# Kernel optimization log

Measured on AMD Instinct MI355X. Metric: run time of the kernel, lower is better.

## Reference

```python
import jax, jax.numpy as jnp
import numpy as np

H = 768
NH = 12
HD = 64
R = 4
SCALING = 8.0 / 4.0  # lora_alpha / r


def setup_inputs() -> dict:
    key = jax.random.key(0)
    ks = jax.random.split(key, 16)
    B, T = 16, 512
    s = 0.02
    x = jax.random.normal(ks[0], (B, T, H), dtype=jnp.float32)
    mask = jax.random.randint(ks[1], (B, T), 0, 2, dtype=jnp.int32)
    return {
        "x": x,
        "mask": mask,
        "Wq": jax.random.normal(ks[2], (H, H), jnp.float32) * s,
        "bq": jnp.zeros((H,), jnp.float32),
        "Aq": jax.random.normal(ks[3], (R, H), jnp.float32) * s,
        "Bq": jax.random.normal(ks[4], (H, R), jnp.float32) * s,
        "Wk": jax.random.normal(ks[5], (H, H), jnp.float32) * s,
        "bk": jnp.zeros((H,), jnp.float32),
        "Wv": jax.random.normal(ks[6], (H, H), jnp.float32) * s,
        "bv": jnp.zeros((H,), jnp.float32),
        "Av": jax.random.normal(ks[7], (R, H), jnp.float32) * s,
        "Bv": jax.random.normal(ks[8], (H, R), jnp.float32) * s,
        "Wo": jax.random.normal(ks[9], (H, H), jnp.float32) * s,
        "bo": jnp.zeros((H,), jnp.float32),
    }


def _lora_linear(x, W, b, A, Bm):
    # base: x @ W^T + b ; lora: (x @ A^T) @ B^T * scaling (dropout inactive at eval)
    return x @ W.T + b + (x @ A.T) @ Bm.T * SCALING


def reference(x, mask, Wq, bq, Aq, Bq, Wk, bk, Wv, bv, Av, Bv, Wo, bo):
    B, T, _ = x.shape
    q = _lora_linear(x, Wq, bq, Aq, Bq).reshape(B, T, NH, HD).transpose(0, 2, 1, 3)
    k = (x @ Wk.T + bk).reshape(B, T, NH, HD).transpose(0, 2, 1, 3)
    v = _lora_linear(x, Wv, bv, Av, Bv).reshape(B, T, NH, HD).transpose(0, 2, 1, 3)
    # [B, NH, T, T]
    scores = jnp.einsum("bhqd,bhkd->bhqk", q, k) / jnp.sqrt(jnp.float32(HD))
    m = (mask == 0)[:, None, None, :]  # mask key positions where mask==0
    scores = jnp.where(m, jnp.float32(-1e9), scores)
    attn = jax.nn.softmax(scores, axis=-1)  # dropout inactive at eval
    out = jnp.einsum("bhqk,bhkd->bhqd", attn, v)
    out = out.transpose(0, 2, 1, 3).reshape(B, T, H)
    return out @ Wo.T + bo
```

## Files before the change

### kernel.cpp

```cpp
#include <hip/hip_runtime.h>
#include <stdint.h>

#define H 768
#define NHEAD 12
#define HDIM 64
#define BATCH 16
#define TSEQ 512
#define BT (BATCH*TSEQ)
#define C3 (3*H)
#define LDQK 1536

typedef __attribute__((ext_vector_type(8))) short short8;
typedef __attribute__((ext_vector_type(4))) float floatx4;
typedef unsigned short u16;

__device__ __forceinline__ u16 f2bf(float f) {
    union { float f; unsigned int u; } v; v.f = f;
    unsigned int u = v.u;
    return (u16)((u + 0x7FFFu + ((u >> 16) & 1u)) >> 16);
}

__device__ __forceinline__ void async_ld16(const void* g, void* l) {
    __builtin_amdgcn_global_load_lds((__attribute__((address_space(1))) void*)g,
                                     (__attribute__((address_space(3))) void*)l,
                                     16, 0, 0);
}

#define PREP_BLOCKS 9216
#define CVT_BLOCKS  6144
#define CMP_BLOCKS  16
__global__ void prep_kernel(const float* __restrict__ Wq, const float* __restrict__ bq,
                            const float* __restrict__ Aq, const float* __restrict__ Bq,
                            const float* __restrict__ Wk, const float* __restrict__ bk,
                            const float* __restrict__ Wv, const float* __restrict__ bv,
                            const float* __restrict__ Av, const float* __restrict__ Bv,
                            const float* __restrict__ Wo, const float* __restrict__ x,
                            const int* __restrict__ mask,
                            u16* __restrict__ Wall, u16* __restrict__ Wobf,
                            float* __restrict__ bias_all, u16* __restrict__ xb,
                            u16* __restrict__ tokl, int* __restrict__ nvalid)
{
    const int bid = blockIdx.x;
    if (bid >= PREP_BLOCKS + CVT_BLOCKS) {
        const int b = bid - (PREP_BLOCKS + CVT_BLOCKS);
        if (threadIdx.x >= 64) return;
        const int lane = threadIdx.x;
        int base = 0;
        for (int t0 = 0; t0 < TSEQ; t0 += 64) {
            const int mv = mask[b*TSEQ + t0 + lane];
            const unsigned long long bal = __ballot(mv != 0);
            if (mv != 0) {
                const int pre = __popcll(bal & ((1ull << lane) - 1ull));
                tokl[b*TSEQ + base + pre] = (u16)(t0 + lane);
            }
            base += __popcll(bal);
        }
        if (lane == 0) nvalid[b] = base;
        for (int i = base + lane; i < TSEQ; i += 64) tokl[b*TSEQ + i] = 0;
        return;
    }
    if (bid >= PREP_BLOCKS) {
        const int i = ((bid - PREP_BLOCKS) * 256 + threadIdx.x) * 4;
        const float4 v = *(const float4*)(x + i);
        u16 o[4] = { f2bf(v.x), f2bf(v.y), f2bf(v.z), f2bf(v.w) };
        *(uint2*)(xb + i) = *(const uint2*)o;
        return;
    }
    const int idx = bid * 256 + threadIdx.x;
    const int r = idx / H;
    const int c = idx - r * H;
    if (r < H) {
        float v = Wq[idx] + 2.0f * (Bq[r*4+0]*Aq[c] + Bq[r*4+1]*Aq[H+c] +
                                    Bq[r*4+2]*Aq[2*H+c] + Bq[r*4+3]*Aq[3*H+c]);
        Wall[idx] = f2bf(v);
    } else if (r < 2*H) {
        Wall[idx] = f2bf(Wk[idx - H*H]);
    } else if (r < 3*H) {
        const int rr = r - 2*H;
        float v = Wv[rr*H + c] + 2.0f * (Bv[rr*4+0]*Av[c] + Bv[rr*4+1]*Av[H+c] +
                                         Bv[rr*4+2]*Av[2*H+c] + Bv[rr*4+3]*Av[3*H+c]);
        Wall[idx] = f2bf(v);
    } else {
        Wobf[idx - 3*H*H] = f2bf(Wo[idx - 3*H*H]);
    }
    if (idx < C3) {
        bias_all[idx] = (idx < H) ? bq[idx] : (idx < 2*H ? bk[idx - H] : bv[idx - 2*H]);
    }
}

template<int MODE, int TM, int NB, int MB, int MAP, int GB>
__global__ __launch_bounds__(256)
void gemm_bt(const u16* __restrict__ A, const u16* __restrict__ Bw,
             const float* __restrict__ bias, void* __restrict__ Cout,
             const u16* __restrict__ tokl, const int* __restrict__ nvalid,
             int K, int ldc)
{
    constexpr int MT = TM / 32;
    __shared__ u16 Ablk[TM * 64];
    __shared__ u16 Bblk[128 * 64];
    const int tid  = threadIdx.x;
    const int wave = tid >> 6;
    const int lane = tid & 63;
    const int quad = lane >> 4;
    const int l16  = lane & 15;

    int m0, n0;
    {
        const int j   = blockIdx.x;
        const int xcd = j & 7;
        const int loc = j >> 3;
        if (MAP == 0) {
            constexpr int Mx = MB / 8;
            const int dm = loc % Mx;
            const int nb = loc / Mx;
            m0 = (xcd + 8*dm) * TM;
            n0 = nb * 128;
        } else {
            const int dm = loc % MB;
            const int nl = loc / MB;
            m0 = dm * TM;
            n0 = (xcd + 8*nl) * 128;
        }
    }

    if (GB) {
        const int b = n0 >> 9;
        if ((n0 & 511) >= ((nvalid[b] + 31) & ~31)) return;
    }

    const int mw = (wave & 1) * (TM / 2);
    const int nw = (wave >> 1) * 64;

    const int r8 = lane >> 3;
    const int kgs = ((lane & 7) ^ r8) * 8;
    const u16* gA = A  + (size_t)(m0 + wave*(TM/4) + r8) * K + kgs;
    const u16* gB = Bw + (size_t)(n0 + wave*32      + r8) * K + kgs;
    const u16* gBp[4];
    if (GB) {
        #pragma unroll
        for (int jj = 0; jj < 4; jj++) {
            const int rb = n0 + wave*32 + jj*8 + r8;
            const int row = (rb & ~511) + (int)tokl[rb];
            gBp[jj] = Bw + (size_t)row * K + kgs;
        }
    }
    u16* lA = Ablk + wave * (TM/4) * 64;
    u16* lB = Bblk + wave * 32 * 64;

    floatx4 acc[MT][4] = {};
    const int sw = l16 & 7;

    for (int k0 = 0; k0 < K; k0 += 64) {
        __syncthreads();
        #pragma unroll
        for (int jj = 0; jj < TM/32; jj++)
            async_ld16(gA + k0 + (size_t)(jj*8) * K, lA + jj*8*64);
        #pragma unroll
        for (int jj = 0; jj < 4; jj++) {
            if (GB) async_ld16(gBp[jj] + k0, lB + jj*8*64);
            else    async_ld16(gB + k0 + (size_t)(jj*8) * K, lB + jj*8*64);
        }
        __syncthreads();
        #pragma unroll
        for (int kk = 0; kk < 2; kk++) {
            short8 af[MT], bfr[4];
            #pragma unroll
            for (int mt = 0; mt < MT; mt++)
                af[mt] = *(const short8*)(Ablk + (mw + mt*16 + l16)*64 + ((quad + 4*kk) ^ sw)*8);
            #pragma unroll
            for (int nt = 0; nt < 4; nt++)
                bfr[nt] = *(const short8*)(Bblk + (nw + nt*16 + l16)*64 + ((quad + 4*kk) ^ sw)*8);
            #pragma unroll
            for (int mt = 0; mt < MT; mt++)
                #pragma unroll
                for (int nt = 0; nt < 4; nt++)
                    acc[mt][nt] = __builtin_amdgcn_mfma_f32_16x16x32_bf16(af[mt], bfr[nt], acc[mt][nt], 0, 0, 0);
        }
    }

    if (MODE == 2) {
        #pragma unroll
        for (int mt = 0; mt < MT; mt++) {
            #pragma unroll
            for (int r = 0; r < 4; r++) {
                const int m  = m0 + mw + mt*16 + quad*4 + r;
                const float bv = bias[m];
                const int hh = m >> 6, d = m & 63;
                #pragma unroll
                for (int nt = 0; nt < 4; nt++) {
                    const int n = n0 + nw + nt*16 + l16;
                    const int b = n >> 9, t = n & 511;
                    ((u16*)Cout)[((size_t)((b*NHEAD + hh)*HDIM + d))*TSEQ + t]
                        = f2bf(acc[mt][nt][r] + bv);
                }
            }
        }
    } else {
        #pragma unroll
        for (int nt = 0; nt < 4; nt++) {
            const int n = n0 + nw + nt*16 + l16;
            const float bv = bias[n];
            #pragma unroll
            for (int mt = 0; mt < MT; mt++) {
                #pragma unroll
                for (int r = 0; r < 4; r++) {
                    const int m = m0 + mw + mt*16 + quad*4 + r;
                    const float v = acc[mt][nt][r] + bv;
                    if (MODE == 1) ((u16*)Cout)[(size_t)m * ldc + n] = f2bf(v);
                    else           ((float*)Cout)[(size_t)m * ldc + n] = v;
                }
            }
        }
    }
}

#define PSTRIDE 40

__global__ __launch_bounds__(256)
void attn_kernel(const u16* __restrict__ qk, const u16* __restrict__ vt,
                 const u16* __restrict__ tokl, const int* __restrict__ nvalid,
                 u16* __restrict__ attn_out)
{
    __shared__ float maskadd[TSEQ];
    __shared__ u16 Kbuf[2][32 * 64];
    __shared__ u16 Vbuf[2][64 * 32];
    __shared__ u16 Pbuf[4][2][16 * PSTRIDE];

    const int qt = blockIdx.x;
    const int bh = blockIdx.y;
    const int b = bh / NHEAD, h = bh - b * NHEAD;
    const int tid  = threadIdx.x;
    const int wave = tid >> 6;
    const int lane = tid & 63;
    const int quad = lane >> 4;
    const int l16  = lane & 15;

    const int nv = nvalid[b];
    const int nt = (nv + 31) >> 5;

    for (int i = tid; i < TSEQ; i += 256)
        maskadd[i] = (i < nv) ? 0.0f : -1e9f;

    const size_t btok = (size_t)b * TSEQ;
    const int q0 = qt * 128 + wave * 32;

    short8 qf[2][2];
    #pragma unroll
    for (int m = 0; m < 2; m++) {
        const u16* qp = qk + (btok + q0 + m*16 + l16) * LDQK + h*HDIM + quad*8;
        qf[m][0] = *(const short8*)qp;
        qf[m][1] = *(const short8*)(qp + 32);
    }

    const u16* vglob = vt + (size_t)bh * HDIM * TSEQ;

    auto stage = [&](int kb, int pp) {
        {
            const int r = lane >> 3;
            const int g = (lane & 7) ^ r;
            const int slot = kb + wave*8 + r;
            const int tk = (int)tokl[btok + slot];
            async_ld16(qk + (btok + tk) * LDQK + H + h*HDIM + g*8,
                       &Kbuf[pp][wave*8*64]);
        }
        {
            const int dr = lane >> 2;
            const int g  = (lane & 3) ^ ((dr >> 1) & 3);
            async_ld16(vglob + (size_t)(wave*16 + dr) * TSEQ + kb + g*8,
                       &Vbuf[pp][wave*16*32]);
        }
    };

    floatx4 o[2][4] = {};
    float lsum[2][4] = {};

    auto compute = [&](int kb, int pp) {
        const u16* Kb_ = Kbuf[pp];
        const u16* Vb_ = Vbuf[pp];
        short8 kf[2][2];
        #pragma unroll
        for (int t = 0; t < 2; t++)
            #pragma unroll
            for (int h2 = 0; h2 < 2; h2++)
                kf[t][h2] = *(const short8*)(Kb_ + (t*16 + l16)*64 + (((h2*4 + quad) ^ (l16 & 7))*8));
        short8 vf[4];
        #pragma unroll
        for (int dt = 0; dt < 4; dt++)
            vf[dt] = *(const short8*)(Vb_ + (dt*16 + l16)*32 + ((quad ^ ((l16 >> 1) & 3))*8));

        floatx4 s[2][2];
        #pragma unroll
        for (int m = 0; m < 2; m++)
            #pragma unroll
            for (int t = 0; t < 2; t++) {
                floatx4 acc = {0.f, 0.f, 0.f, 0.f};
                acc = __builtin_amdgcn_mfma_f32_16x16x32_bf16(qf[m][0], kf[t][0], acc, 0, 0, 0);
                acc = __builtin_amdgcn_mfma_f32_16x16x32_bf16(qf[m][1], kf[t][1], acc, 0, 0, 0);
                s[m][t] = acc;
            }
        const float m0 = maskadd[kb + l16];
        const float m1 = maskadd[kb + 16 + l16];
        #pragma unroll
        for (int m = 0; m < 2; m++) {
            u16* Pw = Pbuf[wave][m];
            #pragma unroll
            for (int r = 0; r < 4; r++) {
                const float p0 = __expf(s[m][0][r] * 0.125f + m0);
                const float p1 = __expf(s[m][1][r] * 0.125f + m1);
                lsum[m][r] += p0 + p1;
                Pw[(quad*4 + r) * PSTRIDE + l16]      = f2bf(p0);
                Pw[(quad*4 + r) * PSTRIDE + 16 + l16] = f2bf(p1);
            }
        }
        #pragma unroll
        for (int m = 0; m < 2; m++) {
            const short8 pa = *(const short8*)(Pbuf[wave][m] + l16 * PSTRIDE + quad*8);
            #pragma unroll
            for (int dt = 0; dt < 4; dt++)
                o[m][dt] = __builtin_amdgcn_mfma_f32_16x16x32_bf16(pa, vf[dt], o[m][dt], 0, 0, 0);
        }
    };

    stage(0, 0);
    for (int it = 0; it < nt; it++) {
        __syncthreads();
        if (it < nt - 1) stage((it + 1) * 32, (it + 1) & 1);
        compute(it * 32, it & 1);
    }

    #pragma unroll
    for (int m = 0; m < 2; m++) {
        float inv[4];
        #pragma unroll
        for (int r = 0; r < 4; r++) {
            float l = lsum[m][r];
            l += __shfl_xor(l, 1);
            l += __shfl_xor(l, 2);
            l += __shfl_xor(l, 4);
            l += __shfl_xor(l, 8);
            inv[r] = 1.0f / l;
        }
        #pragma unroll
        for (int dt = 0; dt < 4; dt++)
            #pragma unroll
            for (int r = 0; r < 4; r++) {
                const int q = q0 + m*16 + quad*4 + r;
                attn_out[(btok + q) * H + h*HDIM + dt*16 + l16] = f2bf(o[m][dt][r] * inv[r]);
            }
    }
}

extern "C" void kernel_launch(void* const* d_in, const int* in_sizes, int n_in,
                              void* d_out, int out_size, void* d_ws, size_t ws_size,
                              hipStream_t stream)
{
    const float* x   = (const float*)d_in[0];
    const int* mask  = (const int*)d_in[1];
    const float* Wq  = (const float*)d_in[2];
    const float* bq  = (const float*)d_in[3];
    const float* Aq  = (const float*)d_in[4];
    const float* Bq  = (const float*)d_in[5];
    const float* Wk  = (const float*)d_in[6];
    const float* bk  = (const float*)d_in[7];
    const float* Wv  = (const float*)d_in[8];
    const float* bv  = (const float*)d_in[9];
    const float* Av  = (const float*)d_in[10];
    const float* Bv  = (const float*)d_in[11];
    const float* Wo  = (const float*)d_in[12];
    const float* bo  = (const float*)d_in[13];

    char* ws = (char*)d_ws;
    u16*   xb      = (u16*)  (ws);
    u16*   Wall    = (u16*)  (ws + 12582912);
    u16*   Wobf    = (u16*)  (ws + 16121856);
    float* biasall = (float*)(ws + 17301504);
    u16*   qk      = (u16*)  (ws + 17310720);
    u16*   vt      = (u16*)  (ws + 42476544);
    u16*   attn_o  = (u16*)  (ws + 55059456);

    int* nvalid = (int*)((char*)d_out + 25149376);
    u16* tokl   = (u16*)((char*)d_out + 25149440);

    prep_kernel<<<PREP_BLOCKS + CVT_BLOCKS + CMP_BLOCKS, 256, 0, stream>>>(
        Wq, bq, Aq, Bq, Wk, bk, Wv, bv, Av, Bv, Wo, x, mask,
        Wall, Wobf, biasall, xb, tokl, nvalid);
    gemm_bt<1,128,12,64,0,0><<<12*64, 256, 0, stream>>>(xb, Wall, biasall, qk,
                                                        nullptr, nullptr, H, LDQK);
    gemm_bt<2,64,64,12,1,1><<<64*12, 256, 0, stream>>>(Wall + (size_t)2*H*H, xb,
                                                       biasall + 2*H, vt,
                                                       tokl, nvalid, H, 0);
    attn_kernel<<<dim3(TSEQ/128, BATCH*NHEAD), 256, 0, stream>>>(qk, vt, tokl, nvalid, attn_o);
    gemm_bt<0,64,6,128,0,0><<<6*128, 256, 0, stream>>>(attn_o, Wobf, bo, d_out,
                                                       nullptr, nullptr, H, H);
}
```

Before: 195.4 us.

## Fuse Q, K, V projection GEMMs into one launch with compacted K output

Merges the QK GEMM and the V-transpose GEMM into a single kernel that dispatches on block index to three GEMM bodies (Q, K, V), removing one launch and letting all three overlap on the device. K is now produced in compacted token order by gathering rows of x through the token list, and tiles past the valid length are skipped. The attention kernel then reads K contiguously instead of gathering through the token list. This trades a larger shared-memory footprint (the max over all three bodies) and a heterogeneous block mix for less launch overhead, less K GEMM work on masked tokens, and simpler K loads.

Result: faster. 189.6 us (-3.0%).

```diff
diff --git a/kernel.cpp b/kernel.cpp
--- a/kernel.cpp
+++ b/kernel.cpp
@@ -8,7 +8,6 @@
 #define TSEQ 512
 #define BT (BATCH*TSEQ)
 #define C3 (3*H)
-#define LDQK 1536
 
 typedef __attribute__((ext_vector_type(8))) short short8;
 typedef __attribute__((ext_vector_type(4))) float floatx4;
@@ -88,16 +87,14 @@
     }
 }
 
-template<int MODE, int TM, int NB, int MB, int MAP, int GB>
-__global__ __launch_bounds__(256)
-void gemm_bt(const u16* __restrict__ A, const u16* __restrict__ Bw,
-             const float* __restrict__ bias, void* __restrict__ Cout,
-             const u16* __restrict__ tokl, const int* __restrict__ nvalid,
-             int K, int ldc)
+template<int MODE, int TM, int NB, int MB, int MAP, int G>
+__device__ __forceinline__
+void gemm_body(const int j, const u16* __restrict__ A, const u16* __restrict__ Bw,
+               const float* __restrict__ bias, void* __restrict__ Cout,
+               const u16* __restrict__ tokl, const int* __restrict__ nvalid,
+               const int K, const int ldc, u16* __restrict__ Ablk, u16* __restrict__ Bblk)
 {
     constexpr int MT = TM / 32;
-    __shared__ u16 Ablk[TM * 64];
-    __shared__ u16 Bblk[128 * 64];
     const int tid  = threadIdx.x;
     const int wave = tid >> 6;
     const int lane = tid & 63;
@@ -106,7 +103,6 @@
 
     int m0, n0;
     {
-        const int j   = blockIdx.x;
         const int xcd = j & 7;
         const int loc = j >> 3;
         if (MAP == 0) {
@@ -123,9 +119,13 @@
         }
     }
 
-    if (GB) {
+    if (G == 1) {
         const int b = n0 >> 9;
         if ((n0 & 511) >= ((nvalid[b] + 31) & ~31)) return;
+    }
+    if (G == 2) {
+        const int b = m0 >> 9;
+        if ((m0 & 511) >= ((nvalid[b] + 31) & ~31)) return;
     }
 
     const int mw = (wave & 1) * (TM / 2);
@@ -135,8 +135,17 @@
     const int kgs = ((lane & 7) ^ r8) * 8;
     const u16* gA = A  + (size_t)(m0 + wave*(TM/4) + r8) * K + kgs;
     const u16* gB = Bw + (size_t)(n0 + wave*32      + r8) * K + kgs;
+    const u16* gAp[MT];
     const u16* gBp[4];
-    if (GB) {
+    if (G == 2) {
+        #pragma unroll
+        for (int jj = 0; jj < MT; jj++) {
+            const int rs = m0 + wave*(TM/4) + jj*8 + r8;
+            const int row = (rs & ~511) + (int)tokl[rs];
+            gAp[jj] = A + (size_t)row * K + kgs;
+        }
+    }
+    if (G == 1) {
         #pragma unroll
         for (int jj = 0; jj < 4; jj++) {
             const int rb = n0 + wave*32 + jj*8 + r8;
@@ -153,12 +162,14 @@
     for (int k0 = 0; k0 < K; k0 += 64) {
         __syncthreads();
         #pragma unroll
-        for (int jj = 0; jj < TM/32; jj++)
-            async_ld16(gA + k0 + (size_t)(jj*8) * K, lA + jj*8*64);
+        for (int jj = 0; jj < MT; jj++) {
+            if (G == 2) async_ld16(gAp[jj] + k0, lA + jj*8*64);
+            else        async_ld16(gA + k0 + (size_t)(jj*8) * K, lA + jj*8*64);
+        }
         #pragma unroll
         for (int jj = 0; jj < 4; jj++) {
-            if (GB) async_ld16(gBp[jj] + k0, lB + jj*8*64);
-            else    async_ld16(gB + k0 + (size_t)(jj*8) * K, lB + jj*8*64);
+            if (G == 1) async_ld16(gBp[jj] + k0, lB + jj*8*64);
+            else        async_ld16(gB + k0 + (size_t)(jj*8) * K, lB + jj*8*64);
         }
         __syncthreads();
         #pragma unroll
@@ -214,11 +225,45 @@
     }
 }
 
+template<int MODE, int TM, int NB, int MB, int MAP, int G>
+__global__ __launch_bounds__(256)
+void gemm_bt(const u16* __restrict__ A, const u16* __restrict__ Bw,
+             const float* __restrict__ bias, void* __restrict__ Cout,
+             const u16* __restrict__ tokl, const int* __restrict__ nvalid,
+             int K, int ldc)
+{
+    __shared__ u16 Ablk[TM * 64];
+    __shared__ u16 Bblk[128 * 64];
+    gemm_body<MODE,TM,NB,MB,MAP,G>(blockIdx.x, A, Bw, bias, Cout, tokl, nvalid,
+                                   K, ldc, Ablk, Bblk);
+}
+
+__global__ __launch_bounds__(256)
+void gemm_qkv(const u16* __restrict__ xb, const u16* __restrict__ Wall,
+              const float* __restrict__ biasall,
+              u16* __restrict__ qb, u16* __restrict__ kc, u16* __restrict__ vt,
+              const u16* __restrict__ tokl, const int* __restrict__ nvalid)
+{
+    __shared__ u16 Ablk[128 * 64];
+    __shared__ u16 Bblk[128 * 64];
+    const int bid = blockIdx.x;
+    if (bid < 384) {
+        gemm_body<1,128,6,64,0,0>(bid, xb, Wall, biasall, qb,
+                                  nullptr, nullptr, H, H, Ablk, Bblk);
+    } else if (bid < 1152) {
+        gemm_body<1,64,6,128,0,2>(bid - 384, xb, Wall + (size_t)H*H, biasall + H, kc,
+                                  tokl, nvalid, H, H, Ablk, Bblk);
+    } else {
+        gemm_body<2,64,64,12,1,1>(bid - 1152, Wall + (size_t)2*H*H, xb, biasall + 2*H, vt,
+                                  tokl, nvalid, H, 0, Ablk, Bblk);
+    }
+}
+
 #define PSTRIDE 40
 
 __global__ __launch_bounds__(256)
-void attn_kernel(const u16* __restrict__ qk, const u16* __restrict__ vt,
-                 const u16* __restrict__ tokl, const int* __restrict__ nvalid,
+void attn_kernel(const u16* __restrict__ qb, const u16* __restrict__ kc,
+                 const u16* __restrict__ vt, const int* __restrict__ nvalid,
                  u16* __restrict__ attn_out)
 {
     __shared__ float maskadd[TSEQ];
@@ -247,20 +292,19 @@
     short8 qf[2][2];
     #pragma unroll
     for (int m = 0; m < 2; m++) {
-        const u16* qp = qk + (btok + q0 + m*16 + l16) * LDQK + h*HDIM + quad*8;
+        const u16* qp = qb + (btok + q0 + m*16 + l16) * H + h*HDIM + quad*8;
         qf[m][0] = *(const short8*)qp;
         qf[m][1] = *(const short8*)(qp + 32);
     }
 
+    const u16* kglob = kc + btok * H + h*HDIM;
     const u16* vglob = vt + (size_t)bh * HDIM * TSEQ;
 
     auto stage = [&](int kb, int pp) {
         {
             const int r = lane >> 3;
             const int g = (lane & 7) ^ r;
-            const int slot = kb + wave*8 + r;
-            const int tk = (int)tokl[btok + slot];
-            async_ld16(qk + (btok + tk) * LDQK + H + h*HDIM + g*8,
+            async_ld16(kglob + (size_t)(kb + wave*8 + r) * H + g*8,
                        &Kbuf[pp][wave*8*64]);
         }
         {
@@ -374,7 +418,8 @@
     u16*   Wall    = (u16*)  (ws + 12582912);
     u16*   Wobf    = (u16*)  (ws + 16121856);
     float* biasall = (float*)(ws + 17301504);
-    u16*   qk      = (u16*)  (ws + 17310720);
+    u16*   qb      = (u16*)  (ws + 17310720);
+    u16*   kc      = (u16*)  (ws + 29893632);
     u16*   vt      = (u16*)  (ws + 42476544);
     u16*   attn_o  = (u16*)  (ws + 55059456);
 
@@ -384,12 +429,8 @@
     prep_kernel<<<PREP_BLOCKS + CVT_BLOCKS + CMP_BLOCKS, 256, 0, stream>>>(
         Wq, bq, Aq, Bq, Wk, bk, Wv, bv, Av, Bv, Wo, x, mask,
         Wall, Wobf, biasall, xb, tokl, nvalid);
-    gemm_bt<1,128,12,64,0,0><<<12*64, 256, 0, stream>>>(xb, Wall, biasall, qk,
-                                                        nullptr, nullptr, H, LDQK);
-    gemm_bt<2,64,64,12,1,1><<<64*12, 256, 0, stream>>>(Wall + (size_t)2*H*H, xb,
-                                                       biasall + 2*H, vt,
-                                                       tokl, nvalid, H, 0);
-    attn_kernel<<<dim3(TSEQ/128, BATCH*NHEAD), 256, 0, stream>>>(qk, vt, tokl, nvalid, attn_o);
+    gemm_qkv<<<1920, 256, 0, stream>>>(xb, Wall, biasall, qb, kc, vt, tokl, nvalid);
+    attn_kernel<<<dim3(TSEQ/128, BATCH*NHEAD), 256, 0, stream>>>(qb, kc, vt, nvalid, attn_o);
     gemm_bt<0,64,6,128,0,0><<<6*128, 256, 0, stream>>>(attn_o, Wobf, bo, d_out,
                                                        nullptr, nullptr, H, H);
 }
```
